# Optimization experiments

Measured on AMD Instinct MI355X. Metric: run time of the kernel, lower is better.

Reference implementation:

```python
import jax, jax.numpy as jnp
import numpy as np

N_BATCH = 131072
N_MODES = 32
E_CONST = float(np.e)


def setup_inputs() -> dict:
    key = jax.random.key(0)
    k1, k2 = jax.random.split(key)
    phi = jax.random.normal(k1, (N_BATCH, N_MODES), dtype=jnp.float32)
    Gamma = jax.random.uniform(k2, (N_MODES, N_MODES), dtype=jnp.float32)
    w = jnp.zeros((N_MODES,), dtype=jnp.float32)
    return {"phi": phi, "Gamma": Gamma, "w": w}


def reference(phi, Gamma, w):
    # train=True path: mode_min starts at +inf, so mode_min = per-mode batch min
    M = Gamma.shape[0]
    mode_min = jnp.min(phi, axis=0)                      # [M]
    phic = phi - mode_min[None, :] + E_CONST             # [N, M]
    phic = jnp.maximum(phic, E_CONST)                    # clamp: phi[phi<e] = e

    # symmetric gamma lookup: g(i,j) = Gamma[min(i,j), max(i,j)]
    idx = jnp.arange(M)
    G = jnp.where(idx[:, None] < idx[None, :], Gamma, Gamma.T)  # [M, M]

    # off-diagonal partial energies: phi_i^g * phi_j^(1-g)
    pe_off = phic[:, :, None] ** G[None, :, :] * phic[:, None, :] ** (1.0 - G[None, :, :])  # [N,M,M]
    off_mask = 1.0 - jnp.eye(M, dtype=phic.dtype)
    # diagonal term: (1 + w_i) * phi_i
    mode_energies = jnp.sum(pe_off * off_mask, axis=-1) + (1.0 + w)[None, :] * phic  # [N, M]

    t = 1.0 / np.sqrt(M)
    logits = jax.nn.log_softmax(-t * mode_energies, axis=-1)
    alphas = jnp.exp(logits)
    return alphas, logits
```

## Files before the change

kernel.cpp:

```cpp
#include <hip/hip_runtime.h>
#include <math.h>

#define NB 131072
#define NM 32
#define EC 2.7182818284590452f
#define TS 0.17677669529663687f
#define L2E 1.4426950408889634f
#define LN2F 0.6931471805599453f


#if __has_builtin(__builtin_amdgcn_exp2f)
__device__ __forceinline__ float fexp2(float x) { return __builtin_amdgcn_exp2f(x); }
#else
__device__ __forceinline__ float fexp2(float x) { return exp2f(x); }
#endif
#if __has_builtin(__builtin_amdgcn_logf)
__device__ __forceinline__ float flog2(float x) { return __builtin_amdgcn_logf(x); }
#else
__device__ __forceinline__ float flog2(float x) { return __log2f(x); }
#endif
#if __has_builtin(__builtin_amdgcn_rcpf)
__device__ __forceinline__ float frcp(float x) { return __builtin_amdgcn_rcpf(x); }
#else
__device__ __forceinline__ float frcp(float x) { return 1.0f / x; }
#endif

__global__ __launch_bounds__(256) void k_min(const float* __restrict__ phi,
                                             float* __restrict__ ws) {
    __shared__ float sm[1024];
    const int tid = threadIdx.x;
    const int g = blockIdx.x * 256 + tid;
    const float4* __restrict__ p4 = (const float4*)phi;
    float4 m = p4[g];
    #pragma unroll
    for (int k = 1; k < 16; ++k) {
        float4 v = p4[g + k * 65536];
        m.x = fminf(m.x, v.x); m.y = fminf(m.y, v.y);
        m.z = fminf(m.z, v.z); m.w = fminf(m.w, v.w);
    }
    sm[tid * 4 + 0] = m.x; sm[tid * 4 + 1] = m.y;
    sm[tid * 4 + 2] = m.z; sm[tid * 4 + 3] = m.w;
    __syncthreads();
    #pragma unroll
    for (int s = 128; s >= 8; s >>= 1) {
        if (tid < s) {
            sm[tid * 4 + 0] = fminf(sm[tid * 4 + 0], sm[(tid + s) * 4 + 0]);
            sm[tid * 4 + 1] = fminf(sm[tid * 4 + 1], sm[(tid + s) * 4 + 1]);
            sm[tid * 4 + 2] = fminf(sm[tid * 4 + 2], sm[(tid + s) * 4 + 2]);
            sm[tid * 4 + 3] = fminf(sm[tid * 4 + 3], sm[(tid + s) * 4 + 3]);
        }
        __syncthreads();
    }
    if (tid < 8) {
        #pragma unroll
        for (int s2 = 0; s2 < 4; ++s2)
            ws[2048 + blockIdx.x * 32 + tid * 4 + s2] = sm[tid * 4 + s2];
    }
}

__global__ __launch_bounds__(256) void k_prep(const float* __restrict__ Gamma,
                                              float* __restrict__ ws) {
    __shared__ float sm[256];
    const int tid = threadIdx.x;
    const int c = tid & 31, h = tid >> 5;
    float m = INFINITY;
    #pragma unroll
    for (int b = 0; b < 32; ++b)
        m = fminf(m, ws[2048 + (h * 32 + b) * 32 + c]);
    sm[tid] = m;
    __syncthreads();
    if (tid < 32) {
        float mm = sm[tid];
        #pragma unroll
        for (int g2 = 1; g2 < 8; ++g2) mm = fminf(mm, sm[g2 * 32 + tid]);
        ws[1024 + tid] = mm - EC;
    }
    #pragma unroll
    for (int k = 0; k < 4; ++k) {
        int idx = tid + 256 * k;
        int i = idx >> 5, j = idx & 31;
        int lo = min(i, j), hi = i + j - lo;
        ws[idx] = Gamma[lo * 32 + hi];
    }
}

__global__ __launch_bounds__(256, 2) void k_main(const float* __restrict__ phi,
                                                 const float* __restrict__ w,
                                                 const float* __restrict__ ws,
                                                 float* __restrict__ out) {
    __shared__ float sL[32 * 256];
    const int tid = threadIdx.x;
    const size_t row = (size_t)blockIdx.x * 256 + tid;
    const float* __restrict__ pr = phi + row * NM;
    const float* __restrict__ mme = ws + 1024;

    float L[32];
    #pragma unroll
    for (int k = 0; k < 8; ++k) {
        float4 v = ((const float4*)pr)[k];
        float a0 = fmaxf(v.x - mme[4 * k + 0], EC);
        float a1 = fmaxf(v.y - mme[4 * k + 1], EC);
        float a2 = fmaxf(v.z - mme[4 * k + 2], EC);
        float a3 = fmaxf(v.w - mme[4 * k + 3], EC);
        L[4 * k + 0] = flog2(a0); L[4 * k + 1] = flog2(a1);
        L[4 * k + 2] = flog2(a2); L[4 * k + 3] = flog2(a3);
    }
    #pragma unroll
    for (int j = 0; j < 32; ++j) sL[j * 256 + tid] = L[j];

    #pragma unroll 1
    for (int it = 0; it < 32; it += 4) {
        const float Li0 = sL[(it + 0) * 256 + tid];
        const float Li1 = sL[(it + 1) * 256 + tid];
        const float Li2 = sL[(it + 2) * 256 + tid];
        const float Li3 = sL[(it + 3) * 256 + tid];
        const float w0 = w[it + 0], w1 = w[it + 1];
        const float w2 = w[it + 2], w3 = w[it + 3];
        const float* __restrict__ g0 = ws + (it + 0) * 32;
        const float* __restrict__ g1 = ws + (it + 1) * 32;
        const float* __restrict__ g2 = ws + (it + 2) * 32;
        const float* __restrict__ g3 = ws + (it + 3) * 32;
        float a00 = 0.f, a01 = 0.f, a02 = 0.f, a03 = 0.f;
        float a10 = 0.f, a11 = 0.f, a12 = 0.f, a13 = 0.f;
        float a20 = 0.f, a21 = 0.f, a22 = 0.f, a23 = 0.f;
        float a30 = 0.f, a31 = 0.f, a32 = 0.f, a33 = 0.f;
        #pragma unroll
        for (int j = 0; j < 32; j += 4) {
            const float lj0 = L[j + 0], lj1 = L[j + 1];
            const float lj2 = L[j + 2], lj3 = L[j + 3];
            a00 += fexp2(fmaf(g0[j + 0], Li0 - lj0, lj0));
            a01 += fexp2(fmaf(g0[j + 1], Li0 - lj1, lj1));
            a02 += fexp2(fmaf(g0[j + 2], Li0 - lj2, lj2));
            a03 += fexp2(fmaf(g0[j + 3], Li0 - lj3, lj3));
            a10 += fexp2(fmaf(g1[j + 0], Li1 - lj0, lj0));
            a11 += fexp2(fmaf(g1[j + 1], Li1 - lj1, lj1));
            a12 += fexp2(fmaf(g1[j + 2], Li1 - lj2, lj2));
            a13 += fexp2(fmaf(g1[j + 3], Li1 - lj3, lj3));
            a20 += fexp2(fmaf(g2[j + 0], Li2 - lj0, lj0));
            a21 += fexp2(fmaf(g2[j + 1], Li2 - lj1, lj1));
            a22 += fexp2(fmaf(g2[j + 2], Li2 - lj2, lj2));
            a23 += fexp2(fmaf(g2[j + 3], Li2 - lj3, lj3));
            a30 += fexp2(fmaf(g3[j + 0], Li3 - lj0, lj0));
            a31 += fexp2(fmaf(g3[j + 1], Li3 - lj1, lj1));
            a32 += fexp2(fmaf(g3[j + 2], Li3 - lj2, lj2));
            a33 += fexp2(fmaf(g3[j + 3], Li3 - lj3, lj3));
        }
        sL[(it + 0) * 256 + tid] =
            -TS * ((((a00 + a01) + (a02 + a03))) + w0 * fexp2(Li0));
        sL[(it + 1) * 256 + tid] =
            -TS * ((((a10 + a11) + (a12 + a13))) + w1 * fexp2(Li1));
        sL[(it + 2) * 256 + tid] =
            -TS * ((((a20 + a21) + (a22 + a23))) + w2 * fexp2(Li2));
        sL[(it + 3) * 256 + tid] =
            -TS * ((((a30 + a31) + (a32 + a33))) + w3 * fexp2(Li3));
    }

    float xs[32];
    #pragma unroll
    for (int i = 0; i < 32; ++i) xs[i] = sL[i * 256 + tid];
    float m = xs[0];
    #pragma unroll
    for (int i = 1; i < 32; ++i) m = fmaxf(m, xs[i]);
    float p[32];
    float s = 0.f;
    #pragma unroll
    for (int i = 0; i < 32; ++i) { p[i] = fexp2((xs[i] - m) * L2E); s += p[i]; }
    const float inv = frcp(s);
    const float lns = flog2(s) * LN2F;

    float* __restrict__ oa = out + row * NM;
    float* __restrict__ ol = out + (size_t)NB * NM + row * NM;
    #pragma unroll
    for (int k = 0; k < 8; ++k) {
        float4 a4 = { p[4 * k + 0] * inv, p[4 * k + 1] * inv,
                      p[4 * k + 2] * inv, p[4 * k + 3] * inv };
        float4 l4 = { (xs[4 * k + 0] - m) - lns, (xs[4 * k + 1] - m) - lns,
                      (xs[4 * k + 2] - m) - lns, (xs[4 * k + 3] - m) - lns };
        ((float4*)oa)[k] = a4;
        ((float4*)ol)[k] = l4;
    }
}

extern "C" void kernel_launch(void* const* d_in, const int* in_sizes, int n_in,
                              void* d_out, int out_size, void* d_ws, size_t ws_size,
                              hipStream_t stream) {
    (void)in_sizes; (void)n_in; (void)out_size; (void)ws_size;
    const float* phi   = (const float*)d_in[0];
    const float* Gamma = (const float*)d_in[1];
    const float* w     = (const float*)d_in[2];
    float* out = (float*)d_out;
    float* wsf = (float*)d_ws;

    k_min<<<256, 256, 0, stream>>>(phi, wsf);
    k_prep<<<1, 256, 0, stream>>>(Gamma, wsf);
    k_main<<<512, 256, 0, stream>>>(phi, w, wsf, out);
}
```

Baseline: 113.6 us.

## Keep per-row state in registers and traverse mode pairs symmetrically

The per-row LDS staging buffer and the rolled 4-row blocked loop are removed. The main loop is replaced by a fully unrolled upper-triangle loop over mode pairs, with all accumulators held in registers. Each pair updates both acc[i] and acc[j], and the diagonal term (1+w)*phi is folded in exactly at init. This drops the 32 redundant diagonal exp2 calls and all LDS traffic. The cost is a very large unrolled body (about 992 exp2 plus scalar Gamma loads), which risks instruction-cache pressure and higher register use.

```diff
diff --git a/kernel.cpp b/kernel.cpp
--- a/kernel.cpp
+++ b/kernel.cpp
@@ -88,76 +88,42 @@
                                                  const float* __restrict__ w,
                                                  const float* __restrict__ ws,
                                                  float* __restrict__ out) {
-    __shared__ float sL[32 * 256];
     const int tid = threadIdx.x;
     const size_t row = (size_t)blockIdx.x * 256 + tid;
     const float* __restrict__ pr = phi + row * NM;
     const float* __restrict__ mme = ws + 1024;
 
     float L[32];
+    float acc[32];
     #pragma unroll
     for (int k = 0; k < 8; ++k) {
         float4 v = ((const float4*)pr)[k];
-        float a0 = fmaxf(v.x - mme[4 * k + 0], EC);
-        float a1 = fmaxf(v.y - mme[4 * k + 1], EC);
-        float a2 = fmaxf(v.z - mme[4 * k + 2], EC);
-        float a3 = fmaxf(v.w - mme[4 * k + 3], EC);
-        L[4 * k + 0] = flog2(a0); L[4 * k + 1] = flog2(a1);
-        L[4 * k + 2] = flog2(a2); L[4 * k + 3] = flog2(a3);
+        float p0 = fmaxf(v.x - mme[4 * k + 0], EC);
+        float p1 = fmaxf(v.y - mme[4 * k + 1], EC);
+        float p2 = fmaxf(v.z - mme[4 * k + 2], EC);
+        float p3 = fmaxf(v.w - mme[4 * k + 3], EC);
+        L[4 * k + 0] = flog2(p0); L[4 * k + 1] = flog2(p1);
+        L[4 * k + 2] = flog2(p2); L[4 * k + 3] = flog2(p3);
+        acc[4 * k + 0] = fmaf(w[4 * k + 0], p0, p0);
+        acc[4 * k + 1] = fmaf(w[4 * k + 1], p1, p1);
+        acc[4 * k + 2] = fmaf(w[4 * k + 2], p2, p2);
+        acc[4 * k + 3] = fmaf(w[4 * k + 3], p3, p3);
     }
+
     #pragma unroll
-    for (int j = 0; j < 32; ++j) sL[j * 256 + tid] = L[j];
-
-    #pragma unroll 1
-    for (int it = 0; it < 32; it += 4) {
-        const float Li0 = sL[(it + 0) * 256 + tid];
-        const float Li1 = sL[(it + 1) * 256 + tid];
-        const float Li2 = sL[(it + 2) * 256 + tid];
-        const float Li3 = sL[(it + 3) * 256 + tid];
-        const float w0 = w[it + 0], w1 = w[it + 1];
-        const float w2 = w[it + 2], w3 = w[it + 3];
-        const float* __restrict__ g0 = ws + (it + 0) * 32;
-        const float* __restrict__ g1 = ws + (it + 1) * 32;
-        const float* __restrict__ g2 = ws + (it + 2) * 32;
-        const float* __restrict__ g3 = ws + (it + 3) * 32;
-        float a00 = 0.f, a01 = 0.f, a02 = 0.f, a03 = 0.f;
-        float a10 = 0.f, a11 = 0.f, a12 = 0.f, a13 = 0.f;
-        float a20 = 0.f, a21 = 0.f, a22 = 0.f, a23 = 0.f;
-        float a30 = 0.f, a31 = 0.f, a32 = 0.f, a33 = 0.f;
+    for (int i = 0; i < 31; ++i) {
         #pragma unroll
-        for (int j = 0; j < 32; j += 4) {
-            const float lj0 = L[j + 0], lj1 = L[j + 1];
-            const float lj2 = L[j + 2], lj3 = L[j + 3];
-            a00 += fexp2(fmaf(g0[j + 0], Li0 - lj0, lj0));
-            a01 += fexp2(fmaf(g0[j + 1], Li0 - lj1, lj1));
-            a02 += fexp2(fmaf(g0[j + 2], Li0 - lj2, lj2));
-            a03 += fexp2(fmaf(g0[j + 3], Li0 - lj3, lj3));
-            a10 += fexp2(fmaf(g1[j + 0], Li1 - lj0, lj0));
-            a11 += fexp2(fmaf(g1[j + 1], Li1 - lj1, lj1));
-            a12 += fexp2(fmaf(g1[j + 2], Li1 - lj2, lj2));
-            a13 += fexp2(fmaf(g1[j + 3], Li1 - lj3, lj3));
-            a20 += fexp2(fmaf(g2[j + 0], Li2 - lj0, lj0));
-            a21 += fexp2(fmaf(g2[j + 1], Li2 - lj1, lj1));
-            a22 += fexp2(fmaf(g2[j + 2], Li2 - lj2, lj2));
-            a23 += fexp2(fmaf(g2[j + 3], Li2 - lj3, lj3));
-            a30 += fexp2(fmaf(g3[j + 0], Li3 - lj0, lj0));
-            a31 += fexp2(fmaf(g3[j + 1], Li3 - lj1, lj1));
-            a32 += fexp2(fmaf(g3[j + 2], Li3 - lj2, lj2));
-            a33 += fexp2(fmaf(g3[j + 3], Li3 - lj3, lj3));
+        for (int j = i + 1; j < 32; ++j) {
+            const float g = ws[i * 32 + j];
+            const float d = L[i] - L[j];
+            acc[i] += fexp2(fmaf(g, d, L[j]));
+            acc[j] += fexp2(fmaf(g, -d, L[i]));
         }
-        sL[(it + 0) * 256 + tid] =
-            -TS * ((((a00 + a01) + (a02 + a03))) + w0 * fexp2(Li0));
-        sL[(it + 1) * 256 + tid] =
-            -TS * ((((a10 + a11) + (a12 + a13))) + w1 * fexp2(Li1));
-        sL[(it + 2) * 256 + tid] =
-            -TS * ((((a20 + a21) + (a22 + a23))) + w2 * fexp2(Li2));
-        sL[(it + 3) * 256 + tid] =
-            -TS * ((((a30 + a31) + (a32 + a33))) + w3 * fexp2(Li3));
     }
 
     float xs[32];
     #pragma unroll
-    for (int i = 0; i < 32; ++i) xs[i] = sL[i * 256 + tid];
+    for (int i = 0; i < 32; ++i) xs[i] = -TS * acc[i];
     float m = xs[0];
     #pragma unroll
     for (int i = 1; i < 32; ++i) m = fmaxf(m, xs[i]);
```

Measured after the change: 105.2 us. -7.4%, faster.
